# Kernel optimization log

Hardware: AMD Instinct MI355X
Metric: run time of the kernel (lower is better)

The kernel has to match this reference:

```python
import jax, jax.numpy as jnp
import numpy as np

BS, C, H, W = 16, 64, 128, 128
NC = 80          # num classes (hardcoded 80 in original via expand(-1, 80, -1))
TOPK = 128
TAU = 0.07
EPS = 1e-12      # F.normalize eps


def setup_inputs() -> dict:
    key = jax.random.key(0)
    k1, k2, k3, k4 = jax.random.split(key, 4)
    feat = jax.random.normal(k1, (BS, C, H, W), dtype=jnp.float32)
    score = jax.random.uniform(k2, (BS, NC, H, W), dtype=jnp.float32)
    # hm: GT heatmap with exactly one 1.0 peak per (batch, class) for ~half the classes
    pos = jax.random.randint(k3, (BS, NC), 0, H * W)
    present = jax.random.bernoulli(k4, 0.5, (BS, NC)).astype(jnp.float32)
    b = jnp.arange(BS)[:, None]
    c = jnp.arange(NC)[None, :]
    hm = jnp.zeros((BS, NC, H * W), jnp.float32).at[b, c, pos].set(present)
    hm = hm.reshape(BS, NC, H, W)
    return {"feat": feat, "score": score, "hm": hm}


def reference(feat, score, hm):
    bs, c, h, w = feat.shape
    nc = hm.shape[1]
    hw = h * w
    score = jax.lax.stop_gradient(score)  # score.detach()

    # F.normalize(feat, dim=1)
    feat = feat / jnp.maximum(jnp.linalg.norm(feat, axis=1, keepdims=True), EPS)

    # q: feature at the hm==1 peak of each present class (one peak per (b,cls))
    peak = (hm == 1.0).astype(feat.dtype)                       # [bs,nc,h,w]
    q = jnp.einsum('bnhw,bchw->bnc', peak, feat)                # [bs,nc,c]
    class_mask = (peak.sum(axis=(2, 3)) > 0).astype(feat.dtype)  # [bs,nc]

    # k0: hm-weighted pooled feature per class, L2-normalized
    k0 = jnp.einsum('bchw,bnhw->bnc', feat, hm)                 # [bs,nc,c]
    k0 = k0 / jnp.maximum(jnp.linalg.norm(k0, axis=-1, keepdims=True), EPS)

    # mask score: zero at GT locations and for absent classes
    hm_free = (hm.sum(axis=1) == 0).astype(score.dtype)         # [bs,h,w]
    score = score * hm_free[:, None] * class_mask[:, :, None, None]

    max_values = score.max(axis=1).reshape(bs, hw)              # [bs,hw]
    class_indices = score.argmax(axis=1).reshape(bs, hw)        # [bs,hw]
    topk_values, topk_indices = jax.lax.top_k(max_values, TOPK)  # [bs,topk]
    k_all_mask_t = (topk_values > 0).astype(feat.dtype)         # [bs,topk]
    topk_class = jnp.take_along_axis(class_indices, topk_indices, axis=1)  # [bs,topk]

    feat_flat = feat.reshape(bs, c, hw)
    k_top = jnp.take_along_axis(feat_flat, topk_indices[:, None, :], axis=2)  # [bs,c,topk]
    k_top = k_top.transpose(0, 2, 1)                            # [bs,topk,c]

    # pseudo heatmap: 0.9 at selected (class, pos) pairs with positive score
    b_idx = jnp.arange(bs)[:, None]
    pseudo_hm = jnp.zeros((bs, nc, hw), feat.dtype).at[
        b_idx, topk_class, topk_indices].set(k_all_mask_t * 0.9)
    pseudo_hm = pseudo_hm.reshape(bs, nc, h, w)

    # positive mask: selected positions whose pseudo class matches the query class
    class_ids = jnp.arange(nc, dtype=feat.dtype)
    target = jnp.where(class_mask[:, :, None] == 1, class_ids[None, :, None], -1.0)  # [bs,nc,1]
    k_mask_top = (target == topk_class[:, None, :].astype(feat.dtype)).astype(feat.dtype)
    k_mask_top = k_mask_top * k_all_mask_t[:, None, :]          # [bs,nc,topk]
    k0_mask = class_mask[:, :, None] * jnp.eye(nc, dtype=feat.dtype)  # [bs,nc,nc]

    k_all = jnp.concatenate([k_top, k0], axis=1)                # [bs,topk+nc,c]
    k_mask = jnp.concatenate([k_mask_top, k0_mask], axis=-1)    # [bs,nc,topk+nc]
    k_all_mask = jnp.concatenate([k_all_mask_t, class_mask], axis=-1)  # [bs,topk+nc]

    sim = jnp.exp(jnp.einsum('bnc,bkc->bnk', q, k_all) / TAU)   # [bs,nc,topk+nc]
    sim_sum = (sim * k_all_mask[:, None, :]).sum(-1, keepdims=True)
    sim_sum = jnp.where(sim_sum == 0, 1.0, sim_sum)
    logit = jnp.where(k_mask > 0, sim / sim_sum, 1.0)
    log_loss = (jnp.log(logit) * k_mask).sum(-1)                # [bs,nc]
    num = k_mask.sum(-1)
    num = jnp.where(num == 0, 1.0, num)
    count = class_mask.sum()
    loss = ((log_loss / num) * class_mask).sum() / count
    return (-loss, pseudo_hm)
```

## Files before the change

kernel.cpp:

```cpp
#include <hip/hip_runtime.h>
#include <math.h>

#define BS 16
#define C 64
#define H 128
#define W 128
#define HW (H*W)
#define NC 80
#define TOPK 128
#define KALL (TOPK+NC)
#define TAU 0.07f
#define EPSN 1e-12f

__global__ __launch_bounds__(1024) void k_peak(const float* __restrict__ hm,
                                               int* __restrict__ peak_pos) {
    __shared__ int wmax[16];
    int bn = blockIdx.x, t = threadIdx.x;
    int lane = t & 63, wid = t >> 6;
    const float4* p = (const float4*)(hm + (size_t)bn * HW);
    int found = -1;
    #pragma unroll
    for (int j = 0; j < 4; ++j) {
        int gi = j * 1024 + t;
        float4 v = p[gi];
        int base = gi * 4;
        if (v.x == 1.0f) found = base;
        if (v.y == 1.0f) found = base + 1;
        if (v.z == 1.0f) found = base + 2;
        if (v.w == 1.0f) found = base + 3;
    }
    #pragma unroll
    for (int off = 1; off < 64; off <<= 1) found = max(found, __shfl_xor(found, off));
    if (lane == 0) wmax[wid] = found;
    __syncthreads();
    if (t == 0) {
        int m = wmax[0];
        #pragma unroll
        for (int i = 1; i < 16; ++i) m = max(m, wmax[i]);
        peak_pos[bn] = m;
    }
}

__global__ void k_max(const float* __restrict__ score, const int* __restrict__ peak_pos,
                      float* __restrict__ maxv, int* __restrict__ clsidx) {
    __shared__ int pk[NC];
    int b = blockIdx.y;
    int g = blockIdx.x * blockDim.x + threadIdx.x;
    if (threadIdx.x < NC) pk[threadIdx.x] = peak_pos[b * NC + threadIdx.x];
    __syncthreads();
    const float4* sb = (const float4*)(score + (size_t)b * NC * HW);
    int p0 = g * 4;
    int pp0 = pk[0];
    float m0 = (pp0 >= 0) ? 1.0f : 0.0f;
    float4 v0 = sb[g];
    float bx = v0.x * m0, by = v0.y * m0, bz = v0.z * m0, bw = v0.w * m0;
    int ix = 0, iy = 0, iz = 0, iw = 0;
    bool pe0 = (pp0 == p0), pe1 = (pp0 == p0 + 1), pe2 = (pp0 == p0 + 2), pe3 = (pp0 == p0 + 3);
    #pragma unroll 8
    for (int n = 1; n < NC; ++n) {
        int pp = pk[n];
        float m = (pp >= 0) ? 1.0f : 0.0f;
        float4 v = sb[(size_t)n * (HW / 4) + g];
        float vx = v.x * m, vy = v.y * m, vz = v.z * m, vw = v.w * m;
        if (vx > bx) { bx = vx; ix = n; }
        if (vy > by) { by = vy; iy = n; }
        if (vz > bz) { bz = vz; iz = n; }
        if (vw > bw) { bw = vw; iw = n; }
        pe0 |= (pp == p0); pe1 |= (pp == p0 + 1); pe2 |= (pp == p0 + 2); pe3 |= (pp == p0 + 3);
    }
    if (pe0) { bx = 0.0f; ix = 0; }
    if (pe1) { by = 0.0f; iy = 0; }
    if (pe2) { bz = 0.0f; iz = 0; }
    if (pe3) { bw = 0.0f; iw = 0; }
    ((float4*)maxv)[(size_t)b * (HW / 4) + g] = make_float4(bx, by, bz, bw);
    ((int4*)clsidx)[(size_t)b * (HW / 4) + g] = make_int4(ix, iy, iz, iw);
}

__global__ __launch_bounds__(1024) void k_topk(const float* __restrict__ maxv,
                                               const int* __restrict__ clsidx,
                                               float* __restrict__ topkv,
                                               int* __restrict__ topki,
                                               int* __restrict__ topkc) {
    __shared__ unsigned int hist[2048];
    __shared__ unsigned int wtot[16];
    __shared__ unsigned int woff[16];
    __shared__ unsigned int s_pref;
    __shared__ int s_rank;
    __shared__ unsigned int s_bin;
    __shared__ unsigned int s_above;

    int b = blockIdx.x, t = threadIdx.x;
    int lane = t & 63, wid = t >> 6;
    unsigned int key[16];
    const float4* mv4 = (const float4*)(maxv + (size_t)b * HW);
    #pragma unroll
    for (int j4 = 0; j4 < 4; ++j4) {
        float4 v = mv4[t * 4 + j4];
        key[j4 * 4 + 0] = __float_as_uint(v.x);
        key[j4 * 4 + 1] = __float_as_uint(v.y);
        key[j4 * 4 + 2] = __float_as_uint(v.z);
        key[j4 * 4 + 3] = __float_as_uint(v.w);
    }

    if (t == 0) { s_pref = 0u; s_rank = TOPK; }

    const int shifts[3] = {21, 10, 0};
    const int widths[3] = {11, 11, 10};

    for (int rnd = 0; rnd < 3; ++rnd) {
        int sh = shifts[rnd], w = widths[rnd];
        unsigned mask = (1u << w) - 1u;
        hist[t] = 0u; hist[t + 1024] = 0u;
        __syncthreads();
        unsigned pref = s_pref;
        int hiShift = sh + w;
        #pragma unroll
        for (int j = 0; j < 16; ++j) {
            unsigned k = key[j];
            bool ok = (rnd == 0) || ((k >> hiShift) == pref);
            if (ok) atomicAdd(&hist[(k >> sh) & mask], 1u);
        }
        __syncthreads();
        unsigned p = hist[2 * t] + hist[2 * t + 1];
        unsigned s = p;
        #pragma unroll
        for (int off = 1; off < 64; off <<= 1) {
            unsigned o = __shfl_down(s, off);
            if (lane + off < 64) s += o;
        }
        if (lane == 0) wtot[wid] = s;
        __syncthreads();
        if (wid == 0) {
            unsigned vv = (lane < 16) ? wtot[lane] : 0u;
            unsigned ss = vv;
            #pragma unroll
            for (int off = 1; off < 64; off <<= 1) {
                unsigned o = __shfl_down(ss, off);
                if (lane + off < 64) ss += o;
            }
            if (lane < 16) woff[lane] = ss - vv;
        }
        __syncthreads();
        unsigned S_t = s + woff[wid];
        unsigned S_next = S_t - p;
        int r = s_rank;
        if ((int)S_t >= r && (int)S_next < r) {
            unsigned hi = hist[2 * t + 1];
            if ((int)(S_next + hi) >= r) { s_bin = 2u * t + 1u; s_above = S_next; }
            else                         { s_bin = 2u * t;      s_above = S_next + hi; }
        }
        __syncthreads();
        if (t == 0) {
            s_pref = (s_pref << w) | s_bin;
            s_rank = s_rank - (int)s_above;
        }
        __syncthreads();
    }
    unsigned K = s_pref;
    int need_eq = s_rank;
    int cnt_gt = TOPK - need_eq;

    int cg = 0, ce = 0;
    #pragma unroll
    for (int j = 0; j < 16; ++j) { cg += (key[j] > K); ce += (key[j] == K); }
    unsigned v = ((unsigned)cg << 16) | (unsigned)ce;
    unsigned sc = v;
    #pragma unroll
    for (int off = 1; off < 64; off <<= 1) {
        unsigned o = __shfl_up(sc, off);
        if (lane >= off) sc += o;
    }
    if (lane == 63) wtot[wid] = sc;
    __syncthreads();
    if (wid == 0) {
        unsigned vv = (lane < 16) ? wtot[lane] : 0u;
        unsigned ss = vv;
        #pragma unroll
        for (int off = 1; off < 64; off <<= 1) {
            unsigned o = __shfl_up(ss, off);
            if (lane >= off) ss += o;
        }
        if (lane < 16) woff[lane] = ss - vv;
    }
    __syncthreads();
    unsigned ex = (sc - v) + woff[wid];
    int pg = (int)(ex >> 16);
    int pe = (int)(ex & 0xffffu);
    int lg = 0, le = 0;
    #pragma unroll
    for (int j = 0; j < 16; ++j) {
        unsigned k = key[j];
        int slot = -1;
        if (k > K) { slot = pg + lg; ++lg; }
        else if (k == K) { int er = pe + le; ++le; if (er < need_eq) slot = cnt_gt + er; }
        if (slot >= 0) {
            int idx = t * 16 + j;
            topkv[b * TOPK + slot] = __uint_as_float(k);
            topki[b * TOPK + slot] = idx;
            topkc[b * TOPK + slot] = clsidx[(size_t)b * HW + idx];
        }
    }
}

__global__ void k_gather(const float* __restrict__ feat, const int* __restrict__ peak_pos,
                         const int* __restrict__ topki, float* k_all, float* qv) {
    int bk = blockIdx.x;
    int b = bk / KALL, k = bk % KALL, c = threadIdx.x;
    int pos;
    if (k < TOPK) {
        pos = topki[b * TOPK + k];
    } else {
        int n = k - TOPK;
        int pp = peak_pos[b * NC + n];
        if (pp < 0) {
            k_all[((size_t)b * KALL + k) * C + c] = 0.0f;
            qv[((size_t)b * NC + n) * C + c] = 0.0f;
            return;
        }
        pos = pp;
    }
    float v = feat[((size_t)b * C + c) * HW + pos];
    float ss = v * v;
    #pragma unroll
    for (int off = 1; off < 64; off <<= 1) ss += __shfl_xor(ss, off);
    float qc = v / fmaxf(sqrtf(ss), EPSN);
    if (k < TOPK) {
        k_all[((size_t)b * KALL + k) * C + c] = qc;
    } else {
        int n = k - TOPK;
        qv[((size_t)b * NC + n) * C + c] = qc;
        float qq = qc * qc;
        #pragma unroll
        for (int off = 1; off < 64; off <<= 1) qq += __shfl_xor(qq, off);
        k_all[((size_t)b * KALL + k) * C + c] = qc / fmaxf(sqrtf(qq), EPSN);
    }
}

__global__ void k_loss(const float* __restrict__ k_all, const float* __restrict__ qv,
                       const int* __restrict__ peak_pos, const float* __restrict__ topkv,
                       const int* __restrict__ topkc, float* loss_bn) {
    __shared__ float qs[C];
    __shared__ float r1[256];
    __shared__ float r2[256];
    __shared__ float s_simsum, s_num;
    int bn = blockIdx.x;
    int b = bn / NC, n = bn % NC, t = threadIdx.x;
    if (peak_pos[bn] < 0) { if (t == 0) loss_bn[bn] = 0.0f; return; }
    if (t < C) qs[t] = qv[(size_t)bn * C + t];
    __syncthreads();
    float sim = 0.0f, kam = 0.0f, km = 0.0f;
    if (t < KALL) {
        const float* kr = k_all + ((size_t)b * KALL + t) * C;
        float dot = 0.0f;
        for (int c2 = 0; c2 < C; ++c2) dot += qs[c2] * kr[c2];
        sim = expf(dot / TAU);
        if (t < TOPK) {
            float posm = (topkv[b * TOPK + t] > 0.0f) ? 1.0f : 0.0f;
            kam = posm;
            km = (topkc[b * TOPK + t] == n) ? posm : 0.0f;
        } else {
            int j = t - TOPK;
            kam = (peak_pos[b * NC + j] >= 0) ? 1.0f : 0.0f;
            km = (j == n) ? 1.0f : 0.0f;
        }
    }
    r1[t] = sim * kam;
    r2[t] = km;
    __syncthreads();
    for (int s = 128; s > 0; s >>= 1) {
        if (t < s) { r1[t] += r1[t + s]; r2[t] += r2[t + s]; }
        __syncthreads();
    }
    if (t == 0) {
        float ss = r1[0];
        s_simsum = (ss == 0.0f) ? 1.0f : ss;
        s_num = (r2[0] == 0.0f) ? 1.0f : r2[0];
    }
    __syncthreads();
    r1[t] = (km > 0.0f) ? logf(sim / s_simsum) : 0.0f;
    __syncthreads();
    for (int s = 128; s > 0; s >>= 1) {
        if (t < s) r1[t] += r1[t + s];
        __syncthreads();
    }
    if (t == 0) loss_bn[bn] = r1[0] / s_num;
}

__global__ void k_scatter(const float* __restrict__ topkv, const int* __restrict__ topki,
                          const int* __restrict__ topkc, float* out) {
    int i = blockIdx.x * blockDim.x + threadIdx.x;
    if (i >= BS * TOPK) return;
    int b = i / TOPK;
    if (topkv[i] > 0.0f)
        out[1 + ((size_t)b * NC + topkc[i]) * HW + topki[i]] = 0.9f;
}

__global__ void k_final(const float* __restrict__ loss_bn, const int* __restrict__ peak_pos,
                        float* out) {
    __shared__ float r1[256];
    __shared__ float r2[256];
    int t = threadIdx.x;
    float s = 0.0f, cnt = 0.0f;
    for (int i = t; i < BS * NC; i += 256) {
        s += loss_bn[i];
        cnt += (peak_pos[i] >= 0) ? 1.0f : 0.0f;
    }
    r1[t] = s; r2[t] = cnt;
    __syncthreads();
    for (int st = 128; st > 0; st >>= 1) {
        if (t < st) { r1[t] += r1[t + st]; r2[t] += r2[t + st]; }
        __syncthreads();
    }
    if (t == 0) out[0] = -(r1[0] / r2[0]);
}

extern "C" void kernel_launch(void* const* d_in, const int* in_sizes, int n_in,
                              void* d_out, int out_size, void* d_ws, size_t ws_size,
                              hipStream_t stream) {
    const float* feat  = (const float*)d_in[0];
    const float* score = (const float*)d_in[1];
    const float* hm    = (const float*)d_in[2];
    float* out = (float*)d_out;

    char* ws = (char*)d_ws;
    size_t off = 0;
    auto alloc = [&](size_t bytes) -> void* {
        void* p = ws + off;
        off += (bytes + 255) & ~(size_t)255;
        return p;
    };
    int*   peak_pos = (int*)  alloc((size_t)BS * NC * 4);
    float* maxv     = (float*)alloc((size_t)BS * HW * 4);
    int*   clsidx   = (int*)  alloc((size_t)BS * HW * 4);
    float* topkv    = (float*)alloc((size_t)BS * TOPK * 4);
    int*   topki    = (int*)  alloc((size_t)BS * TOPK * 4);
    int*   topkc    = (int*)  alloc((size_t)BS * TOPK * 4);
    float* k_all    = (float*)alloc((size_t)BS * KALL * C * 4);
    float* qv       = (float*)alloc((size_t)BS * NC * C * 4);
    float* loss_bn  = (float*)alloc((size_t)BS * NC * 4);

    hipMemsetAsync(d_out, 0, (size_t)out_size * sizeof(float), stream);
    k_peak<<<BS * NC, 1024, 0, stream>>>(hm, peak_pos);
    dim3 gmax(HW / 4 / 256, BS);
    k_max<<<gmax, 256, 0, stream>>>(score, peak_pos, maxv, clsidx);
    k_topk<<<BS, 1024, 0, stream>>>(maxv, clsidx, topkv, topki, topkc);
    k_gather<<<BS * KALL, 64, 0, stream>>>(feat, peak_pos, topki, k_all, qv);
    k_loss<<<BS * NC, 256, 0, stream>>>(k_all, qv, peak_pos, topkv, topkc, loss_bn);
    k_scatter<<<(BS * TOPK + 255) / 256, 256, 0, stream>>>(topkv, topki, topkc, out);
    k_final<<<1, 256, 0, stream>>>(loss_bn, peak_pos, out);
}
```

Measured before the change: 100.3 us.

## Fuse gather into topk and merge loss, output write and reduction

Folds the feature gather into the top-k kernel, which records selected positions in a per-batch byte map. A single combined kernel then computes the per-class losses, writes the full pseudo-heatmap output directly from the map (replacing the memset and scatter), and does the final reduction in the last block via an atomic counter. This removes several launches and a separate full-output memset pass. In exchange the gather runs in only one block per batch, which lowers its parallelism.

```diff
diff --git a/kernel.cpp b/kernel.cpp
--- a/kernel.cpp
+++ b/kernel.cpp
@@ -11,6 +11,10 @@
 #define KALL (TOPK+NC)
 #define TAU 0.07f
 #define EPSN 1e-12f
+#define OUT_N 20971521
+#define NCHW (NC*HW)
+#define LOSSBLK (BS*NC)
+#define WBLK 5120
 
 __global__ __launch_bounds__(1024) void k_peak(const float* __restrict__ hm,
                                                int* __restrict__ peak_pos) {
@@ -76,11 +80,16 @@
     ((int4*)clsidx)[(size_t)b * (HW / 4) + g] = make_int4(ix, iy, iz, iw);
 }
 
-__global__ __launch_bounds__(1024) void k_topk(const float* __restrict__ maxv,
-                                               const int* __restrict__ clsidx,
-                                               float* __restrict__ topkv,
-                                               int* __restrict__ topki,
-                                               int* __restrict__ topkc) {
+__global__ __launch_bounds__(1024) void k_topk_gather(const float* __restrict__ maxv,
+                                                      const int* __restrict__ clsidx,
+                                                      const float* __restrict__ feat,
+                                                      const int* __restrict__ peak_pos,
+                                                      float* __restrict__ topkv,
+                                                      int* __restrict__ topkc,
+                                                      unsigned char* __restrict__ map,
+                                                      float* __restrict__ k_all,
+                                                      float* __restrict__ qv,
+                                                      int* __restrict__ counter) {
     __shared__ unsigned int hist[2048];
     __shared__ unsigned int wtot[16];
     __shared__ unsigned int woff[16];
@@ -88,9 +97,20 @@
     __shared__ int s_rank;
     __shared__ unsigned int s_bin;
     __shared__ unsigned int s_above;
+    __shared__ int s_ki[TOPK];
+    __shared__ int s_pk[NC];
 
     int b = blockIdx.x, t = threadIdx.x;
     int lane = t & 63, wid = t >> 6;
+
+    if (b == 0 && t == 0) *counter = 0;
+    {
+        unsigned int* mz = (unsigned int*)(map + (size_t)b * HW);
+        #pragma unroll
+        for (int j = 0; j < 4; ++j) mz[j * 1024 + t] = 0u;
+    }
+    if (t < NC) s_pk[t] = peak_pos[b * NC + t];
+
     unsigned int key[16];
     const float4* mv4 = (const float4*)(maxv + (size_t)b * HW);
     #pragma unroll
@@ -195,123 +215,161 @@
         else if (k == K) { int er = pe + le; ++le; if (er < need_eq) slot = cnt_gt + er; }
         if (slot >= 0) {
             int idx = t * 16 + j;
+            int cls = clsidx[(size_t)b * HW + idx];
             topkv[b * TOPK + slot] = __uint_as_float(k);
-            topki[b * TOPK + slot] = idx;
-            topkc[b * TOPK + slot] = clsidx[(size_t)b * HW + idx];
+            topkc[b * TOPK + slot] = cls;
+            s_ki[slot] = idx;
+            if (__uint_as_float(k) > 0.0f)
+                map[(size_t)b * HW + idx] = (unsigned char)(cls + 1);
+        }
+    }
+    __syncthreads();
+
+    for (int p13 = 0; p13 < 13; ++p13) {
+        int pi = p13 * 16 + wid;
+        int pos = (pi < TOPK) ? s_ki[pi] : s_pk[pi - TOPK];
+        int c = lane;
+        if (pos < 0) {
+            k_all[((size_t)b * KALL + pi) * C + c] = 0.0f;
+            qv[((size_t)b * NC + (pi - TOPK)) * C + c] = 0.0f;
+            continue;
+        }
+        float fv = feat[((size_t)b * C + c) * HW + pos];
+        float ss = fv * fv;
+        #pragma unroll
+        for (int off = 1; off < 64; off <<= 1) ss += __shfl_xor(ss, off);
+        float qc = fv / fmaxf(sqrtf(ss), EPSN);
+        if (pi < TOPK) {
+            k_all[((size_t)b * KALL + pi) * C + c] = qc;
+        } else {
+            qv[((size_t)b * NC + (pi - TOPK)) * C + c] = qc;
+            float qq = qc * qc;
+            #pragma unroll
+            for (int off = 1; off < 64; off <<= 1) qq += __shfl_xor(qq, off);
+            k_all[((size_t)b * KALL + pi) * C + c] = qc / fmaxf(sqrtf(qq), EPSN);
         }
     }
 }
 
-__global__ void k_gather(const float* __restrict__ feat, const int* __restrict__ peak_pos,
-                         const int* __restrict__ topki, float* k_all, float* qv) {
-    int bk = blockIdx.x;
-    int b = bk / KALL, k = bk % KALL, c = threadIdx.x;
-    int pos;
-    if (k < TOPK) {
-        pos = topki[b * TOPK + k];
-    } else {
-        int n = k - TOPK;
-        int pp = peak_pos[b * NC + n];
-        if (pp < 0) {
-            k_all[((size_t)b * KALL + k) * C + c] = 0.0f;
-            qv[((size_t)b * NC + n) * C + c] = 0.0f;
-            return;
-        }
-        pos = pp;
-    }
-    float v = feat[((size_t)b * C + c) * HW + pos];
-    float ss = v * v;
-    #pragma unroll
-    for (int off = 1; off < 64; off <<= 1) ss += __shfl_xor(ss, off);
-    float qc = v / fmaxf(sqrtf(ss), EPSN);
-    if (k < TOPK) {
-        k_all[((size_t)b * KALL + k) * C + c] = qc;
-    } else {
-        int n = k - TOPK;
-        qv[((size_t)b * NC + n) * C + c] = qc;
-        float qq = qc * qc;
-        #pragma unroll
-        for (int off = 1; off < 64; off <<= 1) qq += __shfl_xor(qq, off);
-        k_all[((size_t)b * KALL + k) * C + c] = qc / fmaxf(sqrtf(qq), EPSN);
-    }
-}
-
-__global__ void k_loss(const float* __restrict__ k_all, const float* __restrict__ qv,
-                       const int* __restrict__ peak_pos, const float* __restrict__ topkv,
-                       const int* __restrict__ topkc, float* loss_bn) {
+__global__ __launch_bounds__(256) void k_write_loss(const float* __restrict__ k_all,
+                                                    const float* __restrict__ qv,
+                                                    const int* __restrict__ peak_pos,
+                                                    const float* __restrict__ topkv,
+                                                    const int* __restrict__ topkc,
+                                                    const unsigned char* __restrict__ map,
+                                                    float* __restrict__ loss_bn,
+                                                    int* __restrict__ counter,
+                                                    float* __restrict__ out) {
+    int t = threadIdx.x;
+    if (blockIdx.x >= LOSSBLK) {
+        int zb = blockIdx.x - LOSSBLK;
+        int idx = zb * 256 + t;
+        float4* o4 = (float4*)out;
+        #pragma unroll
+        for (int j = 0; j < 4; ++j) {
+            int g = idx + j * (WBLK * 256);
+            float r[4];
+            #pragma unroll
+            for (int k = 0; k < 4; ++k) {
+                int e = 4 * g + k;
+                float val = 0.0f;
+                if (e > 0) {
+                    int linear = e - 1;
+                    int bb = linear / NCHW;
+                    int rr = linear - bb * NCHW;
+                    int n = rr >> 14;
+                    int pos = rr & (HW - 1);
+                    unsigned char mp = map[((size_t)bb << 14) + pos];
+                    val = (mp == (unsigned char)(n + 1)) ? 0.9f : 0.0f;
+                }
+                r[k] = val;
+            }
+            if (g == 0) {
+                out[1] = r[1]; out[2] = r[2]; out[3] = r[3];
+            } else {
+                o4[g] = make_float4(r[0], r[1], r[2], r[3]);
+            }
+        }
+        if (zb == 0 && t == 0) {
+            int linear = OUT_N - 2;
+            int bb = linear / NCHW;
+            int rr = linear - bb * NCHW;
+            int n = rr >> 14;
+            int pos = rr & (HW - 1);
+            unsigned char mp = map[((size_t)bb << 14) + pos];
+            out[OUT_N - 1] = (mp == (unsigned char)(n + 1)) ? 0.9f : 0.0f;
+        }
+        return;
+    }
     __shared__ float qs[C];
     __shared__ float r1[256];
     __shared__ float r2[256];
     __shared__ float s_simsum, s_num;
+    __shared__ int s_last;
     int bn = blockIdx.x;
-    int b = bn / NC, n = bn % NC, t = threadIdx.x;
-    if (peak_pos[bn] < 0) { if (t == 0) loss_bn[bn] = 0.0f; return; }
-    if (t < C) qs[t] = qv[(size_t)bn * C + t];
-    __syncthreads();
+    int b = bn / NC, n = bn % NC;
+    bool present = (peak_pos[bn] >= 0);
     float sim = 0.0f, kam = 0.0f, km = 0.0f;
-    if (t < KALL) {
-        const float* kr = k_all + ((size_t)b * KALL + t) * C;
-        float dot = 0.0f;
-        for (int c2 = 0; c2 < C; ++c2) dot += qs[c2] * kr[c2];
-        sim = expf(dot / TAU);
-        if (t < TOPK) {
-            float posm = (topkv[b * TOPK + t] > 0.0f) ? 1.0f : 0.0f;
-            kam = posm;
-            km = (topkc[b * TOPK + t] == n) ? posm : 0.0f;
-        } else {
-            int j = t - TOPK;
-            kam = (peak_pos[b * NC + j] >= 0) ? 1.0f : 0.0f;
-            km = (j == n) ? 1.0f : 0.0f;
-        }
-    }
-    r1[t] = sim * kam;
-    r2[t] = km;
-    __syncthreads();
-    for (int s = 128; s > 0; s >>= 1) {
-        if (t < s) { r1[t] += r1[t + s]; r2[t] += r2[t + s]; }
-        __syncthreads();
-    }
-    if (t == 0) {
-        float ss = r1[0];
-        s_simsum = (ss == 0.0f) ? 1.0f : ss;
-        s_num = (r2[0] == 0.0f) ? 1.0f : r2[0];
-    }
-    __syncthreads();
-    r1[t] = (km > 0.0f) ? logf(sim / s_simsum) : 0.0f;
-    __syncthreads();
-    for (int s = 128; s > 0; s >>= 1) {
-        if (t < s) r1[t] += r1[t + s];
-        __syncthreads();
-    }
-    if (t == 0) loss_bn[bn] = r1[0] / s_num;
-}
-
-__global__ void k_scatter(const float* __restrict__ topkv, const int* __restrict__ topki,
-                          const int* __restrict__ topkc, float* out) {
-    int i = blockIdx.x * blockDim.x + threadIdx.x;
-    if (i >= BS * TOPK) return;
-    int b = i / TOPK;
-    if (topkv[i] > 0.0f)
-        out[1 + ((size_t)b * NC + topkc[i]) * HW + topki[i]] = 0.9f;
-}
-
-__global__ void k_final(const float* __restrict__ loss_bn, const int* __restrict__ peak_pos,
-                        float* out) {
-    __shared__ float r1[256];
-    __shared__ float r2[256];
-    int t = threadIdx.x;
-    float s = 0.0f, cnt = 0.0f;
-    for (int i = t; i < BS * NC; i += 256) {
-        s += loss_bn[i];
-        cnt += (peak_pos[i] >= 0) ? 1.0f : 0.0f;
-    }
-    r1[t] = s; r2[t] = cnt;
-    __syncthreads();
-    for (int st = 128; st > 0; st >>= 1) {
-        if (t < st) { r1[t] += r1[t + st]; r2[t] += r2[t + st]; }
-        __syncthreads();
-    }
-    if (t == 0) out[0] = -(r1[0] / r2[0]);
+    if (present) {
+        if (t < C) qs[t] = qv[(size_t)bn * C + t];
+        __syncthreads();
+        if (t < KALL) {
+            const float* kr = k_all + ((size_t)b * KALL + t) * C;
+            float dot = 0.0f;
+            for (int c2 = 0; c2 < C; ++c2) dot += qs[c2] * kr[c2];
+            sim = expf(dot / TAU);
+            if (t < TOPK) {
+                float posm = (topkv[b * TOPK + t] > 0.0f) ? 1.0f : 0.0f;
+                kam = posm;
+                km = (topkc[b * TOPK + t] == n) ? posm : 0.0f;
+            } else {
+                int j = t - TOPK;
+                kam = (peak_pos[b * NC + j] >= 0) ? 1.0f : 0.0f;
+                km = (j == n) ? 1.0f : 0.0f;
+            }
+        }
+        r1[t] = sim * kam;
+        r2[t] = km;
+        __syncthreads();
+        for (int s = 128; s > 0; s >>= 1) {
+            if (t < s) { r1[t] += r1[t + s]; r2[t] += r2[t + s]; }
+            __syncthreads();
+        }
+        if (t == 0) {
+            float ss = r1[0];
+            s_simsum = (ss == 0.0f) ? 1.0f : ss;
+            s_num = (r2[0] == 0.0f) ? 1.0f : r2[0];
+        }
+        __syncthreads();
+        r1[t] = (km > 0.0f) ? logf(sim / s_simsum) : 0.0f;
+        __syncthreads();
+        for (int s = 128; s > 0; s >>= 1) {
+            if (t < s) r1[t] += r1[t + s];
+            __syncthreads();
+        }
+        if (t == 0) loss_bn[bn] = r1[0] / s_num;
+    } else {
+        if (t == 0) loss_bn[bn] = 0.0f;
+    }
+    __threadfence();
+    __syncthreads();
+    if (t == 0) s_last = (atomicAdd(counter, 1) == LOSSBLK - 1) ? 1 : 0;
+    __syncthreads();
+    if (s_last) {
+        __threadfence();
+        float s = 0.0f, cnt = 0.0f;
+        for (int i = t; i < BS * NC; i += 256) {
+            s += loss_bn[i];
+            cnt += (peak_pos[i] >= 0) ? 1.0f : 0.0f;
+        }
+        r1[t] = s; r2[t] = cnt;
+        __syncthreads();
+        for (int st = 128; st > 0; st >>= 1) {
+            if (t < st) { r1[t] += r1[t + st]; r2[t] += r2[t + st]; }
+            __syncthreads();
+        }
+        if (t == 0) out[0] = -(r1[0] / r2[0]);
+    }
 }
 
 extern "C" void kernel_launch(void* const* d_in, const int* in_sizes, int n_in,
@@ -333,19 +391,18 @@
     float* maxv     = (float*)alloc((size_t)BS * HW * 4);
     int*   clsidx   = (int*)  alloc((size_t)BS * HW * 4);
     float* topkv    = (float*)alloc((size_t)BS * TOPK * 4);
-    int*   topki    = (int*)  alloc((size_t)BS * TOPK * 4);
     int*   topkc    = (int*)  alloc((size_t)BS * TOPK * 4);
     float* k_all    = (float*)alloc((size_t)BS * KALL * C * 4);
     float* qv       = (float*)alloc((size_t)BS * NC * C * 4);
     float* loss_bn  = (float*)alloc((size_t)BS * NC * 4);
-
-    hipMemsetAsync(d_out, 0, (size_t)out_size * sizeof(float), stream);
+    unsigned char* map = (unsigned char*)alloc((size_t)BS * HW);
+    int*   counter  = (int*)  alloc(256);
+
     k_peak<<<BS * NC, 1024, 0, stream>>>(hm, peak_pos);
     dim3 gmax(HW / 4 / 256, BS);
     k_max<<<gmax, 256, 0, stream>>>(score, peak_pos, maxv, clsidx);
-    k_topk<<<BS, 1024, 0, stream>>>(maxv, clsidx, topkv, topki, topkc);
-    k_gather<<<BS * KALL, 64, 0, stream>>>(feat, peak_pos, topki, k_all, qv);
-    k_loss<<<BS * NC, 256, 0, stream>>>(k_all, qv, peak_pos, topkv, topkc, loss_bn);
-    k_scatter<<<(BS * TOPK + 255) / 256, 256, 0, stream>>>(topkv, topki, topkc, out);
-    k_final<<<1, 256, 0, stream>>>(loss_bn, peak_pos, out);
+    k_topk_gather<<<BS, 1024, 0, stream>>>(maxv, clsidx, feat, peak_pos,
+                                           topkv, topkc, map, k_all, qv, counter);
+    k_write_loss<<<LOSSBLK + WBLK, 256, 0, stream>>>(k_all, qv, peak_pos, topkv, topkc,
+                                                     map, loss_bn, counter, out);
 }
```

After: 233.1 us. 2.33x slower.
